# Performance work log

Hardware: AMD Instinct MI355X
Metric: run time of the kernel (lower is better)

Reference implementation:

```python
import jax, jax.numpy as jnp
import numpy as np

SIGMA = 1.0

def setup_inputs() -> dict:
    key = jax.random.key(0)
    k1, k2 = jax.random.split(key)
    coords = jax.random.normal(k1, (128, 3), dtype=jnp.float32)        # (N, 3) atom positions
    query_points = jax.random.normal(k2, (262144, 3), dtype=jnp.float32)  # (M, 3) field sample points
    return {"coords": coords, "query_points": query_points}

def reference(coords, query_points):
    # version=1 GNF: gaussian-weighted pairwise differences summed over atoms.
    # diff: (N, M, 3)
    diff = coords[:, None, :] - query_points[None, :, :]
    dist_sq = jnp.sum(diff * diff, axis=-1, keepdims=True)            # (N, M, 1)
    inv_sigma_sq = 1.0 / (SIGMA * SIGMA)
    weights = jnp.exp(-0.5 * dist_sq * inv_sigma_sq) * inv_sigma_sq   # (N, M, 1)
    individual_gradients = diff * weights                              # (N, M, 3)
    return jnp.sum(individual_gradients, axis=0)                       # (M, 3)
```

## Files before the change

kernel.cpp:

```cpp
#include <hip/hip_runtime.h>

#define NATOMS 128
#define QPT 2
#define BLOCK 256

#if defined(__has_builtin)
#if __has_builtin(__builtin_amdgcn_exp2f)
#define EXP2F(x) __builtin_amdgcn_exp2f(x)
#endif
#endif
#ifndef EXP2F
#define EXP2F(x) exp2f(x)
#endif

__global__ __launch_bounds__(BLOCK) void gnf_kernel(
    const float* __restrict__ coords,
    const float* __restrict__ query,
    float* __restrict__ out,
    int M)
{
    __shared__ float4 sA[NATOMS];
    __shared__ float4 sC[NATOMS];

    const float LOG2E = 1.44269504088896340736f;
    const int tid = threadIdx.x;

    if (tid < NATOMS) {
        float cx = coords[tid * 3 + 0];
        float cy = coords[tid * 3 + 1];
        float cz = coords[tid * 3 + 2];
        sA[tid] = make_float4(cx * LOG2E, cy * LOG2E, cz * LOG2E,
                              -0.5f * (cx * cx + cy * cy + cz * cz) * LOG2E);
        sC[tid] = make_float4(cx, cy, cz, 0.0f);
    }
    __syncthreads();

    const int base = (blockIdx.x * BLOCK + tid) * QPT;
    if (base >= M) return;

    float qx[QPT], qy[QPT], qz[QPT], eq[QPT];
    float sw[QPT], sx[QPT], sy[QPT], sz[QPT];

#pragma unroll
    for (int k = 0; k < QPT; ++k) {
        const int m = base + k;
        const float x = query[m * 3 + 0];
        const float y = query[m * 3 + 1];
        const float z = query[m * 3 + 2];
        qx[k] = x; qy[k] = y; qz[k] = z;
        eq[k] = -0.5f * (x * x + y * y + z * z) * LOG2E;
        sw[k] = 0.0f; sx[k] = 0.0f; sy[k] = 0.0f; sz[k] = 0.0f;
    }

#pragma unroll 4
    for (int n = 0; n < NATOMS; ++n) {
        const float4 A = sA[n];
        const float4 C = sC[n];
#pragma unroll
        for (int k = 0; k < QPT; ++k) {
            float t = fmaf(A.x, qx[k], fmaf(A.y, qy[k], fmaf(A.z, qz[k], A.w))) + eq[k];
            float w = EXP2F(t);
            sw[k] += w;
            sx[k] = fmaf(C.x, w, sx[k]);
            sy[k] = fmaf(C.y, w, sy[k]);
            sz[k] = fmaf(C.z, w, sz[k]);
        }
    }

#pragma unroll
    for (int k = 0; k < QPT; ++k) {
        const int m = base + k;
        out[m * 3 + 0] = fmaf(-qx[k], sw[k], sx[k]);
        out[m * 3 + 1] = fmaf(-qy[k], sw[k], sy[k]);
        out[m * 3 + 2] = fmaf(-qz[k], sw[k], sz[k]);
    }
}

extern "C" void kernel_launch(void* const* d_in, const int* in_sizes, int n_in,
                              void* d_out, int out_size, void* d_ws, size_t ws_size,
                              hipStream_t stream) {
    const float* coords = (const float*)d_in[0];
    const float* query  = (const float*)d_in[1];
    float* out = (float*)d_out;
    const int M = in_sizes[1] / 3;
    const int threads = (M + QPT - 1) / QPT;
    const int grid = (threads + BLOCK - 1) / BLOCK;
    gnf_kernel<<<grid, BLOCK, 0, stream>>>(coords, query, out, M);
}
```

Before: 16.16 us.

## Precompute per-atom table in a prep kernel and read it from global memory

```diff
diff --git a/kernel.cpp b/kernel.cpp
--- a/kernel.cpp
+++ b/kernel.cpp
@@ -1,7 +1,6 @@
 #include <hip/hip_runtime.h>
 
 #define NATOMS 128
-#define QPT 2
 #define BLOCK 256
 
 #if defined(__has_builtin)
@@ -13,67 +12,58 @@
 #define EXP2F(x) exp2f(x)
 #endif
 
+__global__ void gnf_prep(const float* __restrict__ coords, float* __restrict__ tbl) {
+    const float LOG2E = 1.44269504088896340736f;
+    int n = threadIdx.x;
+    if (n < NATOMS) {
+        float cx = coords[n * 3 + 0];
+        float cy = coords[n * 3 + 1];
+        float cz = coords[n * 3 + 2];
+        float b  = -0.5f * (cx * cx + cy * cy + cz * cz) * LOG2E;
+        float sb = EXP2F(b);
+        tbl[n * 8 + 0] = cx * LOG2E;
+        tbl[n * 8 + 1] = cy * LOG2E;
+        tbl[n * 8 + 2] = cz * LOG2E;
+        tbl[n * 8 + 3] = sb;
+        tbl[n * 8 + 4] = cx * sb;
+        tbl[n * 8 + 5] = cy * sb;
+        tbl[n * 8 + 6] = cz * sb;
+        tbl[n * 8 + 7] = 0.0f;
+    }
+}
+
 __global__ __launch_bounds__(BLOCK) void gnf_kernel(
-    const float* __restrict__ coords,
+    const float4* __restrict__ tbl,
     const float* __restrict__ query,
     float* __restrict__ out,
     int M)
 {
-    __shared__ float4 sA[NATOMS];
-    __shared__ float4 sC[NATOMS];
+    const float LOG2E = 1.44269504088896340736f;
+    const int m = blockIdx.x * BLOCK + threadIdx.x;
+    if (m >= M) return;
 
-    const float LOG2E = 1.44269504088896340736f;
-    const int tid = threadIdx.x;
+    const float qx = query[m * 3 + 0];
+    const float qy = query[m * 3 + 1];
+    const float qz = query[m * 3 + 2];
+    const float eq = -0.5f * (qx * qx + qy * qy + qz * qz) * LOG2E;
 
-    if (tid < NATOMS) {
-        float cx = coords[tid * 3 + 0];
-        float cy = coords[tid * 3 + 1];
-        float cz = coords[tid * 3 + 2];
-        sA[tid] = make_float4(cx * LOG2E, cy * LOG2E, cz * LOG2E,
-                              -0.5f * (cx * cx + cy * cy + cz * cz) * LOG2E);
-        sC[tid] = make_float4(cx, cy, cz, 0.0f);
-    }
-    __syncthreads();
+    float sw = 0.0f, sx = 0.0f, sy = 0.0f, sz = 0.0f;
 
-    const int base = (blockIdx.x * BLOCK + tid) * QPT;
-    if (base >= M) return;
-
-    float qx[QPT], qy[QPT], qz[QPT], eq[QPT];
-    float sw[QPT], sx[QPT], sy[QPT], sz[QPT];
-
-#pragma unroll
-    for (int k = 0; k < QPT; ++k) {
-        const int m = base + k;
-        const float x = query[m * 3 + 0];
-        const float y = query[m * 3 + 1];
-        const float z = query[m * 3 + 2];
-        qx[k] = x; qy[k] = y; qz[k] = z;
-        eq[k] = -0.5f * (x * x + y * y + z * z) * LOG2E;
-        sw[k] = 0.0f; sx[k] = 0.0f; sy[k] = 0.0f; sz[k] = 0.0f;
+#pragma unroll 8
+    for (int n = 0; n < NATOMS; ++n) {
+        const float4 A = tbl[2 * n + 0];
+        const float4 C = tbl[2 * n + 1];
+        float t = fmaf(A.x, qx, fmaf(A.y, qy, fmaf(A.z, qz, eq)));
+        float w = EXP2F(t);
+        sw = fmaf(A.w, w, sw);
+        sx = fmaf(C.x, w, sx);
+        sy = fmaf(C.y, w, sy);
+        sz = fmaf(C.z, w, sz);
     }
 
-#pragma unroll 4
-    for (int n = 0; n < NATOMS; ++n) {
-        const float4 A = sA[n];
-        const float4 C = sC[n];
-#pragma unroll
-        for (int k = 0; k < QPT; ++k) {
-            float t = fmaf(A.x, qx[k], fmaf(A.y, qy[k], fmaf(A.z, qz[k], A.w))) + eq[k];
-            float w = EXP2F(t);
-            sw[k] += w;
-            sx[k] = fmaf(C.x, w, sx[k]);
-            sy[k] = fmaf(C.y, w, sy[k]);
-            sz[k] = fmaf(C.z, w, sz[k]);
-        }
-    }
-
-#pragma unroll
-    for (int k = 0; k < QPT; ++k) {
-        const int m = base + k;
-        out[m * 3 + 0] = fmaf(-qx[k], sw[k], sx[k]);
-        out[m * 3 + 1] = fmaf(-qy[k], sw[k], sy[k]);
-        out[m * 3 + 2] = fmaf(-qz[k], sw[k], sz[k]);
-    }
+    out[m * 3 + 0] = fmaf(-qx, sw, sx);
+    out[m * 3 + 1] = fmaf(-qy, sw, sy);
+    out[m * 3 + 2] = fmaf(-qz, sw, sz);
 }
 
 extern "C" void kernel_launch(void* const* d_in, const int* in_sizes, int n_in,
@@ -82,8 +72,10 @@
     const float* coords = (const float*)d_in[0];
     const float* query  = (const float*)d_in[1];
     float* out = (float*)d_out;
+    float* tbl = (float*)d_ws;
     const int M = in_sizes[1] / 3;
-    const int threads = (M + QPT - 1) / QPT;
-    const int grid = (threads + BLOCK - 1) / BLOCK;
-    gnf_kernel<<<grid, BLOCK, 0, stream>>>(coords, query, out, M);
+
+    gnf_prep<<<1, NATOMS, 0, stream>>>(coords, tbl);
+    const int grid = (M + BLOCK - 1) / BLOCK;
+    gnf_kernel<<<grid, BLOCK, 0, stream>>>((const float4*)tbl, query, out, M);
 }
```

Result: slower. 20.45 us (+26.5%).
